# Kernel tuning notes

Measured on AMD Instinct MI355X. Metric: run time of the kernel, lower is better.

## Reference

```python
import jax, jax.numpy as jnp
import numpy as np

B, L, S, D = 64, 1024, 8, 128  # batch, seq len, num_snapshots, feat dim


def setup_inputs() -> dict:
    key = jax.random.key(0)
    ks = jax.random.split(key, 12)
    src_ids = jax.random.randint(ks[0], (B, L), 0, 2000, dtype=jnp.int32)
    dst_ids = jax.random.randint(ks[1], (B, L), 0, 2000, dtype=jnp.int32)
    # snapshot ids are 1..S in the original code (indexing uses snaps - 1)
    src_snaps = jax.random.randint(ks[2], (B, L), 1, S + 1, dtype=jnp.int32)
    dst_snaps = jax.random.randint(ks[3], (B, L), 1, S + 1, dtype=jnp.int32)
    def lin(k, fan_in, shape):
        return jax.random.uniform(k, shape, jnp.float32, -1.0, 1.0) / np.sqrt(fan_in)
    params = {
        # AggregateSnapshots MLP: Linear(S, D) -> ReLU -> Linear(D, 2)
        'agg_w1': lin(ks[4], S, (S, D)), 'agg_b1': lin(ks[5], S, (D,)),
        'agg_w2': lin(ks[6], D, (D, 2)), 'agg_b2': lin(ks[7], D, (2,)),
        # neighbor_intersect_encode_layer: Linear(1, D) -> ReLU -> Linear(D, D)
        'enc_w1': lin(ks[8], 1, (1, D)), 'enc_b1': lin(ks[9], 1, (D,)),
        'enc_w2': lin(ks[10], D, (D, D)), 'enc_b2': lin(ks[11], D, (D,)),
    }
    return dict(src_padded_nodes_neighbor_ids=src_ids,
                dst_padded_nodes_neighbor_ids=dst_ids,
                src_padded_nodes_snapshots=src_snaps,
                dst_padded_nodes_snapshots=dst_snaps,
                num_snapshots=S, **params)


def _match_counts(ids_a, sn_a, ids_b, sn_b):
    # counts[i, j] = #{k : ids_b[i,k] == ids_a[i,j] and sn_b[i,k] == sn_a[i,j]}
    eq = (ids_a[:, :, None] == ids_b[:, None, :]) & (sn_a[:, :, None] == sn_b[:, None, :])
    return eq.sum(axis=-1).astype(jnp.float32)  # [B, L]


def _intersects(ids, sn, other_ids, other_sn, num_snapshots):
    self_cnt = _match_counts(ids, sn, ids, sn)            # [B, L]
    cross_cnt = _match_counts(ids, sn, other_ids, other_sn)
    valid = (ids != 0).astype(jnp.float32)                # padding rows stay zero
    oh = jax.nn.one_hot(sn - 1, num_snapshots, dtype=jnp.float32)  # [B, L, S]
    cnts = jnp.stack([self_cnt, cross_cnt], axis=2)       # [B, L, 2]
    return (cnts * valid[:, :, None])[..., None] * oh[:, :, None, :]  # [B, L, 2, S]


def _agg_mlp(x, w1, b1, w2, b2):
    # x: [B, L, 2, S] -> Linear(S,D) -> ReLU -> Linear(D,2) -> reshape(B,L,2,2) -> mean over dim 2
    h = jax.nn.relu(jnp.einsum('blcs,sd->blcd', x, w1) + b1)
    y = jnp.einsum('blcd,de->blce', h, w2) + b2           # [B, L, 2, 2]
    return y.mean(axis=2)                                 # [B, L, 2]


def _encode(y, w1, b1, w2, b2):
    # y: [B, L, 2] -> unsqueeze(-1) -> Linear(1,D) -> ReLU -> Linear(D,D) -> sum over dim 2
    h = jax.nn.relu(y[..., None] * w1[0] + b1)            # [B, L, 2, D]
    z = jnp.einsum('blcd,de->blce', h, w2) + b2
    return z.sum(axis=2)                                  # [B, L, D]


def reference(src_padded_nodes_neighbor_ids, dst_padded_nodes_neighbor_ids,
              src_padded_nodes_snapshots, dst_padded_nodes_snapshots, num_snapshots,
              agg_w1, agg_b1, agg_w2, agg_b2, enc_w1, enc_b1, enc_w2, enc_b2):
    src_int = _intersects(src_padded_nodes_neighbor_ids, src_padded_nodes_snapshots,
                          dst_padded_nodes_neighbor_ids, dst_padded_nodes_snapshots, num_snapshots)
    dst_self_cross = _intersects(dst_padded_nodes_neighbor_ids, dst_padded_nodes_snapshots,
                                 src_padded_nodes_neighbor_ids, src_padded_nodes_snapshots, num_snapshots)
    # dst layout: channel 0 = counts from src list, channel 1 = self counts
    dst_int = dst_self_cross[:, :, ::-1, :]
    src_snap_feat = _agg_mlp(src_int, agg_w1, agg_b1, agg_w2, agg_b2)
    dst_snap_feat = _agg_mlp(dst_int, agg_w1, agg_b1, agg_w2, agg_b2)
    src_feat = _encode(src_snap_feat, enc_w1, enc_b1, enc_w2, enc_b2)
    dst_feat = _encode(dst_snap_feat, enc_w1, enc_b1, enc_w2, enc_b2)
    return (src_feat, dst_feat)
```

## Files before the change

### kernel.cpp

```cpp
#include <hip/hip_runtime.h>


#define LSEQ 1024
#define NBATCH 64
#define DDIM 128
#define NKEYS 16384
#define CMAX 16

__global__ __launch_bounds__(1024) void count_kernel(
    const int* __restrict__ src_ids, const int* __restrict__ dst_ids,
    const int* __restrict__ src_sn,  const int* __restrict__ dst_sn,
    unsigned int* __restrict__ cnt_src, unsigned int* __restrict__ cnt_dst)
{
    __shared__ unsigned int hist[NKEYS];
    const int b = blockIdx.x;
    const int t = threadIdx.x;

    for (int i = t; i < NKEYS; i += 1024) hist[i] = 0u;
    __syncthreads();

    const int base = b * LSEQ;
    const int sid = src_ids[base + t];
    const int ssn = src_sn[base + t];
    const int did = dst_ids[base + t];
    const int dsn = dst_sn[base + t];

    unsigned int skey = (unsigned int)(sid * 8 + ((ssn - 1) & 7));
    unsigned int dkey = (unsigned int)(did * 8 + ((dsn - 1) & 7));
    if (skey >= NKEYS) skey = NKEYS - 1;
    if (dkey >= NKEYS) dkey = NKEYS - 1;

    atomicAdd(&hist[skey], 1u);
    atomicAdd(&hist[dkey], 65536u);
    __syncthreads();

    const unsigned int hs = hist[skey];
    const unsigned int hd = hist[dkey];
    const unsigned int s_self  = hs & 0xffffu, s_cross = hs >> 16;
    const unsigned int d_self  = hd >> 16,     d_cross = hd & 0xffffu;
    const unsigned int sv = (sid != 0) ? 1u : 0u;
    const unsigned int dv = (did != 0) ? 1u : 0u;

    cnt_src[base + t] = (s_self * sv) | ((s_cross * sv) << 11)
                        | ((unsigned int)((ssn - 1) & 7) << 22);
    cnt_dst[base + t] = (d_self * dv) | ((d_cross * dv) << 11)
                        | ((unsigned int)((dsn - 1) & 7) << 22);
}

__global__ __launch_bounds__(128) void table_kernel(
    const float* __restrict__ agg_w1, const float* __restrict__ agg_b1,
    const float* __restrict__ agg_w2, const float* __restrict__ agg_b2,
    const float* __restrict__ enc_w1, const float* __restrict__ enc_b1,
    const float* __restrict__ enc_w2, const float* __restrict__ enc_b2,
    float* __restrict__ table)
{
    const int bx = blockIdx.x;
    const int sn = bx >> 8;
    const int c0 = (bx >> 4) & 15;
    const int c1 = bx & 15;
    const int d  = threadIdx.x;

    __shared__ float red0[DDIM], red1[DDIM], g[DDIM];

    const float w1d = agg_w1[sn * DDIM + d];
    const float b1d = agg_b1[d];
    const float h = fmaxf((float)c0 * w1d + b1d, 0.0f)
                  + fmaxf((float)c1 * w1d + b1d, 0.0f);
    red0[d] = h * agg_w2[d * 2 + 0];
    red1[d] = h * agg_w2[d * 2 + 1];
    __syncthreads();
    for (int s = 64; s > 0; s >>= 1) {
        if (d < s) { red0[d] += red0[d + s]; red1[d] += red1[d + s]; }
        __syncthreads();
    }
    const float y0 = agg_b2[0] + 0.5f * red0[0];
    const float y1 = agg_b2[1] + 0.5f * red1[0];
    __syncthreads();

    const float w1e = enc_w1[d], b1e = enc_b1[d];
    g[d] = fmaxf(y0 * w1e + b1e, 0.0f) + fmaxf(y1 * w1e + b1e, 0.0f);
    __syncthreads();

    float acc = 2.0f * enc_b2[d];
    #pragma unroll 8
    for (int k = 0; k < DDIM; ++k)
        acc += g[k] * enc_w2[k * DDIM + d];
    table[bx * DDIM + d] = acc;
}

__global__ __launch_bounds__(256) void gather_kernel(
    const unsigned int* __restrict__ cnt_src,
    const unsigned int* __restrict__ cnt_dst,
    const float* __restrict__ table,
    const float* __restrict__ agg_w1, const float* __restrict__ agg_b1,
    const float* __restrict__ agg_w2, const float* __restrict__ agg_b2,
    const float* __restrict__ enc_w1, const float* __restrict__ enc_b1,
    const float* __restrict__ enc_w2, const float* __restrict__ enc_b2,
    float* __restrict__ out)
{
    const int gt   = blockIdx.x * 256 + threadIdx.x;
    const int unit = gt >> 5;
    const int q    = gt & 31;
    const int side = unit >> 16;
    const int idx  = unit & 65535;

    const unsigned int packed = side ? cnt_dst[idx] : cnt_src[idx];
    const unsigned int c0 = packed & 0x7FFu;
    const unsigned int c1 = (packed >> 11) & 0x7FFu;
    const unsigned int sn = (packed >> 22) & 7u;

    float4 v;
    if (c0 < CMAX && c1 < CMAX) {
        const float4* src = (const float4*)(table
            + ((sn * 256u + c0 * 16u + c1) * DDIM));
        v = src[q];
    } else {
        float s0 = 0.0f, s1 = 0.0f;
        for (int dd = 0; dd < DDIM; ++dd) {
            const float w1d = agg_w1[sn * DDIM + dd];
            const float b1d = agg_b1[dd];
            const float h = fmaxf((float)c0 * w1d + b1d, 0.0f)
                          + fmaxf((float)c1 * w1d + b1d, 0.0f);
            s0 += h * agg_w2[dd * 2 + 0];
            s1 += h * agg_w2[dd * 2 + 1];
        }
        const float y0 = agg_b2[0] + 0.5f * s0;
        const float y1 = agg_b2[1] + 0.5f * s1;
        float o0 = 2.0f * enc_b2[q * 4 + 0];
        float o1 = 2.0f * enc_b2[q * 4 + 1];
        float o2 = 2.0f * enc_b2[q * 4 + 2];
        float o3 = 2.0f * enc_b2[q * 4 + 3];
        for (int k = 0; k < DDIM; ++k) {
            const float w1e = enc_w1[k], b1e = enc_b1[k];
            const float gk = fmaxf(y0 * w1e + b1e, 0.0f)
                           + fmaxf(y1 * w1e + b1e, 0.0f);
            o0 += gk * enc_w2[k * DDIM + q * 4 + 0];
            o1 += gk * enc_w2[k * DDIM + q * 4 + 1];
            o2 += gk * enc_w2[k * DDIM + q * 4 + 2];
            o3 += gk * enc_w2[k * DDIM + q * 4 + 3];
        }
        v = make_float4(o0, o1, o2, o3);
    }
    ((float4*)out)[gt] = v;
}

extern "C" void kernel_launch(void* const* d_in, const int* in_sizes, int n_in,
                              void* d_out, int out_size, void* d_ws, size_t ws_size,
                              hipStream_t stream)
{
    const int* src_ids = (const int*)d_in[0];
    const int* dst_ids = (const int*)d_in[1];
    const int* src_sn  = (const int*)d_in[2];
    const int* dst_sn  = (const int*)d_in[3];
    const float* agg_w1 = (const float*)d_in[5];
    const float* agg_b1 = (const float*)d_in[6];
    const float* agg_w2 = (const float*)d_in[7];
    const float* agg_b2 = (const float*)d_in[8];
    const float* enc_w1 = (const float*)d_in[9];
    const float* enc_b1 = (const float*)d_in[10];
    const float* enc_w2 = (const float*)d_in[11];
    const float* enc_b2 = (const float*)d_in[12];
    float* out = (float*)d_out;

    unsigned int* cnt_src = (unsigned int*)d_ws;
    unsigned int* cnt_dst = cnt_src + NBATCH * LSEQ;
    float* table = (float*)(cnt_dst + NBATCH * LSEQ);

    count_kernel<<<NBATCH, 1024, 0, stream>>>(src_ids, dst_ids, src_sn, dst_sn,
                                              cnt_src, cnt_dst);
    table_kernel<<<8 * CMAX * CMAX, 128, 0, stream>>>(
        agg_w1, agg_b1, agg_w2, agg_b2, enc_w1, enc_b1, enc_w2, enc_b2, table);
    gather_kernel<<<(2 * NBATCH * LSEQ * 32) / 256, 256, 0, stream>>>(
        cnt_src, cnt_dst, table,
        agg_w1, agg_b1, agg_w2, agg_b2, enc_w1, enc_b1, enc_w2, enc_b2, out);
}
```

Baseline: 112.3 us.

## Fuse histogram counting into gather kernel, moving slow path out of line

Drops the separate count kernel and its workspace round trip. Each batch is now handled by 4 blocks, and every block rebuilds the shared-memory histogram for its batch, then gathers table rows for its quarter of the rows. The slow path becomes a noinline function to keep register pressure off the hot loop. In exchange, the histogram is built four times per batch, and with 256 blocks the gather has fewer, larger blocks than the old launch.

```diff
diff --git a/kernel.cpp b/kernel.cpp
--- a/kernel.cpp
+++ b/kernel.cpp
@@ -6,46 +6,6 @@
 #define DDIM 128
 #define NKEYS 16384
 #define CMAX 16
-
-__global__ __launch_bounds__(1024) void count_kernel(
-    const int* __restrict__ src_ids, const int* __restrict__ dst_ids,
-    const int* __restrict__ src_sn,  const int* __restrict__ dst_sn,
-    unsigned int* __restrict__ cnt_src, unsigned int* __restrict__ cnt_dst)
-{
-    __shared__ unsigned int hist[NKEYS];
-    const int b = blockIdx.x;
-    const int t = threadIdx.x;
-
-    for (int i = t; i < NKEYS; i += 1024) hist[i] = 0u;
-    __syncthreads();
-
-    const int base = b * LSEQ;
-    const int sid = src_ids[base + t];
-    const int ssn = src_sn[base + t];
-    const int did = dst_ids[base + t];
-    const int dsn = dst_sn[base + t];
-
-    unsigned int skey = (unsigned int)(sid * 8 + ((ssn - 1) & 7));
-    unsigned int dkey = (unsigned int)(did * 8 + ((dsn - 1) & 7));
-    if (skey >= NKEYS) skey = NKEYS - 1;
-    if (dkey >= NKEYS) dkey = NKEYS - 1;
-
-    atomicAdd(&hist[skey], 1u);
-    atomicAdd(&hist[dkey], 65536u);
-    __syncthreads();
-
-    const unsigned int hs = hist[skey];
-    const unsigned int hd = hist[dkey];
-    const unsigned int s_self  = hs & 0xffffu, s_cross = hs >> 16;
-    const unsigned int d_self  = hd >> 16,     d_cross = hd & 0xffffu;
-    const unsigned int sv = (sid != 0) ? 1u : 0u;
-    const unsigned int dv = (did != 0) ? 1u : 0u;
-
-    cnt_src[base + t] = (s_self * sv) | ((s_cross * sv) << 11)
-                        | ((unsigned int)((ssn - 1) & 7) << 22);
-    cnt_dst[base + t] = (d_self * dv) | ((d_cross * dv) << 11)
-                        | ((unsigned int)((dsn - 1) & 7) << 22);
-}
 
 __global__ __launch_bounds__(128) void table_kernel(
     const float* __restrict__ agg_w1, const float* __restrict__ agg_b1,
@@ -88,9 +48,43 @@
     table[bx * DDIM + d] = acc;
 }
 
-__global__ __launch_bounds__(256) void gather_kernel(
-    const unsigned int* __restrict__ cnt_src,
-    const unsigned int* __restrict__ cnt_dst,
+__device__ __noinline__ float4 slow_path(
+    unsigned int c0, unsigned int c1, unsigned int sn, int q,
+    const float* __restrict__ agg_w1, const float* __restrict__ agg_b1,
+    const float* __restrict__ agg_w2, const float* __restrict__ agg_b2,
+    const float* __restrict__ enc_w1, const float* __restrict__ enc_b1,
+    const float* __restrict__ enc_w2, const float* __restrict__ enc_b2)
+{
+    float s0 = 0.0f, s1 = 0.0f;
+    for (int dd = 0; dd < DDIM; ++dd) {
+        const float w1d = agg_w1[sn * DDIM + dd];
+        const float b1d = agg_b1[dd];
+        const float h = fmaxf((float)c0 * w1d + b1d, 0.0f)
+                      + fmaxf((float)c1 * w1d + b1d, 0.0f);
+        s0 += h * agg_w2[dd * 2 + 0];
+        s1 += h * agg_w2[dd * 2 + 1];
+    }
+    const float y0 = agg_b2[0] + 0.5f * s0;
+    const float y1 = agg_b2[1] + 0.5f * s1;
+    float o0 = 2.0f * enc_b2[q * 4 + 0];
+    float o1 = 2.0f * enc_b2[q * 4 + 1];
+    float o2 = 2.0f * enc_b2[q * 4 + 2];
+    float o3 = 2.0f * enc_b2[q * 4 + 3];
+    for (int k = 0; k < DDIM; ++k) {
+        const float w1e = enc_w1[k], b1e = enc_b1[k];
+        const float gk = fmaxf(y0 * w1e + b1e, 0.0f)
+                       + fmaxf(y1 * w1e + b1e, 0.0f);
+        o0 += gk * enc_w2[k * DDIM + q * 4 + 0];
+        o1 += gk * enc_w2[k * DDIM + q * 4 + 1];
+        o2 += gk * enc_w2[k * DDIM + q * 4 + 2];
+        o3 += gk * enc_w2[k * DDIM + q * 4 + 3];
+    }
+    return make_float4(o0, o1, o2, o3);
+}
+
+__global__ __launch_bounds__(1024) void fused_kernel(
+    const int* __restrict__ src_ids, const int* __restrict__ dst_ids,
+    const int* __restrict__ src_sn,  const int* __restrict__ dst_sn,
     const float* __restrict__ table,
     const float* __restrict__ agg_w1, const float* __restrict__ agg_b1,
     const float* __restrict__ agg_w2, const float* __restrict__ agg_b2,
@@ -98,50 +92,61 @@
     const float* __restrict__ enc_w2, const float* __restrict__ enc_b2,
     float* __restrict__ out)
 {
-    const int gt   = blockIdx.x * 256 + threadIdx.x;
-    const int unit = gt >> 5;
-    const int q    = gt & 31;
-    const int side = unit >> 16;
-    const int idx  = unit & 65535;
+    __shared__ unsigned int hist[NKEYS];
+    const int b = blockIdx.x >> 2;
+    const int r = blockIdx.x & 3;
+    const int t = threadIdx.x;
 
-    const unsigned int packed = side ? cnt_dst[idx] : cnt_src[idx];
-    const unsigned int c0 = packed & 0x7FFu;
-    const unsigned int c1 = (packed >> 11) & 0x7FFu;
-    const unsigned int sn = (packed >> 22) & 7u;
+    #pragma unroll
+    for (int i = 0; i < NKEYS / 1024; ++i) hist[i * 1024 + t] = 0u;
+    __syncthreads();
 
-    float4 v;
-    if (c0 < CMAX && c1 < CMAX) {
-        const float4* src = (const float4*)(table
-            + ((sn * 256u + c0 * 16u + c1) * DDIM));
-        v = src[q];
-    } else {
-        float s0 = 0.0f, s1 = 0.0f;
-        for (int dd = 0; dd < DDIM; ++dd) {
-            const float w1d = agg_w1[sn * DDIM + dd];
-            const float b1d = agg_b1[dd];
-            const float h = fmaxf((float)c0 * w1d + b1d, 0.0f)
-                          + fmaxf((float)c1 * w1d + b1d, 0.0f);
-            s0 += h * agg_w2[dd * 2 + 0];
-            s1 += h * agg_w2[dd * 2 + 1];
+    const int base = b * LSEQ;
+    {
+        const int sid = src_ids[base + t];
+        const int ssn = src_sn[base + t];
+        const int did = dst_ids[base + t];
+        const int dsn = dst_sn[base + t];
+        unsigned int skey = (unsigned int)(sid * 8 + ((ssn - 1) & 7));
+        unsigned int dkey = (unsigned int)(did * 8 + ((dsn - 1) & 7));
+        if (skey >= NKEYS) skey = NKEYS - 1;
+        if (dkey >= NKEYS) dkey = NKEYS - 1;
+        atomicAdd(&hist[skey], 1u);
+        atomicAdd(&hist[dkey], 65536u);
+    }
+    __syncthreads();
+
+    const int unit = t >> 5;
+    const int q    = t & 31;
+
+    #pragma unroll 1
+    for (int i = 0; i < 16; ++i) {
+        const int row  = r * 512 + i * 32 + unit;
+        const int side = row >> 10;
+        const int l    = row & 1023;
+
+        const int id = side ? dst_ids[base + l] : src_ids[base + l];
+        const int sn = side ? dst_sn[base + l]  : src_sn[base + l];
+
+        unsigned int key = (unsigned int)(id * 8 + ((sn - 1) & 7));
+        if (key >= NKEYS) key = NKEYS - 1;
+        const unsigned int h = hist[key];
+        unsigned int c0 = side ? (h >> 16)     : (h & 0xffffu);
+        unsigned int c1 = side ? (h & 0xffffu) : (h >> 16);
+        if (id == 0) { c0 = 0u; c1 = 0u; }
+        const unsigned int snn = (unsigned int)((sn - 1) & 7);
+
+        float4 v;
+        if (c0 < CMAX && c1 < CMAX) {
+            const float4* srcp = (const float4*)(table
+                + ((snn * 256u + c0 * 16u + c1) * DDIM));
+            v = srcp[q];
+        } else {
+            v = slow_path(c0, c1, snn, q, agg_w1, agg_b1, agg_w2, agg_b2,
+                          enc_w1, enc_b1, enc_w2, enc_b2);
         }
-        const float y0 = agg_b2[0] + 0.5f * s0;
-        const float y1 = agg_b2[1] + 0.5f * s1;
-        float o0 = 2.0f * enc_b2[q * 4 + 0];
-        float o1 = 2.0f * enc_b2[q * 4 + 1];
-        float o2 = 2.0f * enc_b2[q * 4 + 2];
-        float o3 = 2.0f * enc_b2[q * 4 + 3];
-        for (int k = 0; k < DDIM; ++k) {
-            const float w1e = enc_w1[k], b1e = enc_b1[k];
-            const float gk = fmaxf(y0 * w1e + b1e, 0.0f)
-                           + fmaxf(y1 * w1e + b1e, 0.0f);
-            o0 += gk * enc_w2[k * DDIM + q * 4 + 0];
-            o1 += gk * enc_w2[k * DDIM + q * 4 + 1];
-            o2 += gk * enc_w2[k * DDIM + q * 4 + 2];
-            o3 += gk * enc_w2[k * DDIM + q * 4 + 3];
-        }
-        v = make_float4(o0, o1, o2, o3);
+        ((float4*)out)[((size_t)side * (NBATCH * LSEQ) + base + l) * 32 + q] = v;
     }
-    ((float4*)out)[gt] = v;
 }
 
 extern "C" void kernel_launch(void* const* d_in, const int* in_sizes, int n_in,
@@ -162,15 +167,11 @@
     const float* enc_b2 = (const float*)d_in[12];
     float* out = (float*)d_out;
 
-    unsigned int* cnt_src = (unsigned int*)d_ws;
-    unsigned int* cnt_dst = cnt_src + NBATCH * LSEQ;
-    float* table = (float*)(cnt_dst + NBATCH * LSEQ);
+    float* table = (float*)d_ws;
 
-    count_kernel<<<NBATCH, 1024, 0, stream>>>(src_ids, dst_ids, src_sn, dst_sn,
-                                              cnt_src, cnt_dst);
     table_kernel<<<8 * CMAX * CMAX, 128, 0, stream>>>(
         agg_w1, agg_b1, agg_w2, agg_b2, enc_w1, enc_b1, enc_w2, enc_b2, table);
-    gather_kernel<<<(2 * NBATCH * LSEQ * 32) / 256, 256, 0, stream>>>(
-        cnt_src, cnt_dst, table,
+    fused_kernel<<<NBATCH * 4, 1024, 0, stream>>>(
+        src_ids, dst_ids, src_sn, dst_sn, table,
         agg_w1, agg_b1, agg_w2, agg_b2, enc_w1, enc_b1, enc_w2, enc_b2, out);
 }
```

After: 112.8 us. About the same (+0.5%).
